# Performance work log

Hardware: AMD Instinct MI355X
Metric: run time of the kernel (lower is better)

Reference implementation:

```python
import jax, jax.numpy as jnp
import numpy as np

N_NODES = 50000
N_EDGES = 800000
NUM_GRAPHS = 128
FEAT = 128
HID = 64
NUM_LAYERS = 3
OUT = 2
K = 30
LATENT = HID * NUM_LAYERS + 1  # 193 = conv1 kernel size & stride


def _lin(k, i, o):
    s = 1.0 / np.sqrt(i)
    return jax.random.uniform(k, (i, o), jnp.float32, -s, s)


def setup_inputs() -> dict:
    key = jax.random.key(0)
    ks = jax.random.split(key, 16)
    x = jax.random.normal(ks[0], (N_NODES, FEAT), jnp.float32)
    edge_index = jax.random.randint(ks[1], (2, N_EDGES), 0, N_NODES, dtype=jnp.int64)
    batch = jnp.sort(jax.random.randint(ks[2], (N_NODES,), 0, NUM_GRAPHS, dtype=jnp.int64))
    w0 = _lin(ks[3], FEAT, HID); b0 = jnp.zeros((HID,), jnp.float32)
    w1 = _lin(ks[4], HID, HID);  b1 = jnp.zeros((HID,), jnp.float32)
    w2 = _lin(ks[5], HID, HID);  b2 = jnp.zeros((HID,), jnp.float32)
    w3 = _lin(ks[6], HID, 1);    b3 = jnp.zeros((1,), jnp.float32)
    conv1_w = jax.random.normal(ks[7], (16, 1, LATENT), jnp.float32) * (1.0 / np.sqrt(LATENT))
    conv1_b = jnp.zeros((16,), jnp.float32)
    conv2_w = jax.random.normal(ks[8], (32, 16, 5), jnp.float32) * (1.0 / np.sqrt(16 * 5))
    conv2_b = jnp.zeros((32,), jnp.float32)
    dense_dim = (int((K - 2) / 2 + 1) - 5 + 1) * 32  # 352
    lin1_w = _lin(ks[9], dense_dim, 256); lin1_b = jnp.zeros((256,), jnp.float32)
    lin2_w = _lin(ks[10], 256, OUT);      lin2_b = jnp.zeros((OUT,), jnp.float32)
    return dict(x=x, edge_index=edge_index, batch=batch,
                w0=w0, b0=b0, w1=w1, b1=b1, w2=w2, b2=b2, w3=w3, b3=b3,
                conv1_w=conv1_w, conv1_b=conv1_b, conv2_w=conv2_w, conv2_b=conv2_b,
                lin1_w=lin1_w, lin1_b=lin1_b, lin2_w=lin2_w, lin2_b=lin2_b)


def _gcn(h_in, w, b, src, dst, norm, n):
    # GCNConv: out_i = sum_j d_i^-1/2 d_j^-1/2 (x_j W) over A+I, plus bias
    h = h_in @ w
    msg = h[src] * norm[:, None]  # gather over edges (incl. self loops)
    return jax.ops.segment_sum(msg, dst, num_segments=n) + b


def _sort_pool(x, batch, k, g):
    # per-graph descending sort on last channel, top-k, zero-pad
    n, d = x.shape
    order = jnp.lexsort((-x[:, -1], batch))  # primary: batch asc, secondary: last feat desc
    xs, bs = x[order], batch[order]
    counts = jax.ops.segment_sum(jnp.ones((n,), jnp.int32), batch, num_segments=g)
    starts = jnp.cumsum(counts) - counts
    rank = jnp.arange(n) - starts[bs]
    slot = jnp.where(rank < k, rank, k)  # overflow nodes dumped in slot k (discarded)
    out = jnp.zeros((g, k + 1, d), x.dtype).at[bs, slot].set(xs)
    return out[:, :k].reshape(g, k * d)


def _conv1d(z, w, stride):
    return jax.lax.conv_general_dilated(z, w, window_strides=(stride,), padding='VALID',
                                        dimension_numbers=('NCH', 'OIH', 'NCH'))


def reference(x, edge_index, batch, w0, b0, w1, b1, w2, b2, w3, b3,
              conv1_w, conv1_b, conv2_w, conv2_b, lin1_w, lin1_b, lin2_w, lin2_b):
    n = x.shape[0]
    loop = jnp.arange(n, dtype=edge_index.dtype)
    src = jnp.concatenate([edge_index[0], loop])
    dst = jnp.concatenate([edge_index[1], loop])
    deg = jax.ops.segment_sum(jnp.ones_like(src, jnp.float32), dst, num_segments=n)
    dinv = jnp.where(deg > 0, jax.lax.rsqrt(deg), 0.0)
    norm = dinv[src] * dinv[dst]

    h1 = jnp.tanh(_gcn(x,  w0, b0, src, dst, norm, n))
    h2 = jnp.tanh(_gcn(h1, w1, b1, src, dst, norm, n))
    h3 = jnp.tanh(_gcn(h2, w2, b2, src, dst, norm, n))
    h4 = jnp.tanh(_gcn(h3, w3, b3, src, dst, norm, n))
    hcat = jnp.concatenate([h1, h2, h3, h4], axis=-1)  # [N, 193]

    p = _sort_pool(hcat, batch, K, NUM_GRAPHS)  # [G, K*193]
    z = p[:, None, :]                                   # [G, 1, K*193]
    z = jax.nn.relu(_conv1d(z, conv1_w, LATENT) + conv1_b[None, :, None])  # [G,16,K]
    g, c, l = z.shape
    z = z.reshape(g, c, l // 2, 2).max(axis=-1)         # MaxPool1d(2,2) -> [G,16,15]
    z = jax.nn.relu(_conv1d(z, conv2_w, 1) + conv2_b[None, :, None])       # [G,32,11]
    z = z.reshape(g, -1)                                # [G,352]
    z = jax.nn.relu(z @ lin1_w + lin1_b)
    # dropout is identity in eval mode
    return z @ lin2_w + lin2_b
```

## Files before the change

kernel.cpp:

```cpp
#include <hip/hip_runtime.h>
#include <math.h>

#define NGRAPH 128
#define KTOP 30
#define LATENT 193
#define HID 64

__global__ void k_hist_starts(const int* __restrict__ dst, const int* __restrict__ batch,
                              int* edeg, int* starts, int E, int n) {
    int i = blockIdx.x * blockDim.x + threadIdx.x;
    if (i < E) atomicAdd(&edeg[dst[i]], 1);
    if (i < n) {
        int b = batch[i];
        if (i == 0) {
            for (int g = 0; g <= b; g++) starts[g] = 0;
        } else {
            int pb = batch[i - 1];
            for (int g = pb + 1; g <= b; g++) starts[g] = i;
        }
        if (i == n - 1) {
            for (int g = b + 1; g <= NGRAPH; g++) starts[g] = n;
        }
    }
}

__global__ void k_scan1(const int* __restrict__ edeg, int* offs, int* bsum,
                        float* dinv, int n) {
    __shared__ int s[256];
    int t = threadIdx.x;
    int gi = blockIdx.x * 256 + t;
    int v = (gi < n) ? edeg[gi] : 0;
    if (gi < n) dinv[gi] = rsqrtf((float)(v + 1));
    s[t] = v;
    __syncthreads();
    for (int o = 1; o < 256; o <<= 1) {
        int add = (t >= o) ? s[t - o] : 0;
        __syncthreads();
        s[t] += add;
        __syncthreads();
    }
    if (gi < n) offs[gi] = s[t] - v;
    if (t == 255) bsum[blockIdx.x] = s[255];
}

__global__ void k_scan2(int* bsum, int* boff, int nb) {
    __shared__ int s[256];
    int t = threadIdx.x;
    int v = (t < nb) ? bsum[t] : 0;
    s[t] = v;
    __syncthreads();
    for (int o = 1; o < 256; o <<= 1) {
        int add = (t >= o) ? s[t - o] : 0;
        __syncthreads();
        s[t] += add;
        __syncthreads();
    }
    if (t < nb) boff[t] = s[t] - v;
}

__global__ void k_scan3(int* offs, int* next, const int* __restrict__ boff, int n, int E) {
    int gi = blockIdx.x * blockDim.x + threadIdx.x;
    if (gi < n) {
        int v = offs[gi] + boff[gi >> 8];
        offs[gi] = v;
        next[gi] = v;
    }
    if (gi == 0) offs[n] = E;
}

__global__ __launch_bounds__(256) void k_gemm_fill(const float* __restrict__ A,
                                                   const float* __restrict__ W,
                                                   const float* __restrict__ dinv,
                                                   float* __restrict__ Hs,
                                                   int M, int K, int NG,
                                                   const int* __restrict__ src,
                                                   const int* __restrict__ dst,
                                                   int* next, int* __restrict__ csr,
                                                   int E) {
    __shared__ float As[64][17];
    __shared__ float Bs[16][65];
    int bid = blockIdx.x;
    int gemm_id = (bid % 5 == 0) ? bid / 5 : -1;
    if (gemm_id >= 0 && gemm_id < NG) {
        int tid = threadIdx.x;
        int tx = tid & 15, ty = tid >> 4;
        int br = gemm_id * 64;
        float c[4][4] = {};
        for (int k0 = 0; k0 < K; k0 += 16) {
            {
                int idx = tid * 4;
                int r = idx >> 4;
                int kk = idx & 15;
                int grow = br + r;
                float4 v = make_float4(0.f, 0.f, 0.f, 0.f);
                if (grow < M) v = *(const float4*)(A + (size_t)grow * K + k0 + kk);
                As[r][kk + 0] = v.x; As[r][kk + 1] = v.y;
                As[r][kk + 2] = v.z; As[r][kk + 3] = v.w;
            }
            {
                int idx = tid * 4;
                int kk = idx >> 6;
                int col = idx & 63;
                float4 v = *(const float4*)(W + (size_t)(k0 + kk) * 64 + col);
                Bs[kk][col + 0] = v.x; Bs[kk][col + 1] = v.y;
                Bs[kk][col + 2] = v.z; Bs[kk][col + 3] = v.w;
            }
            __syncthreads();
#pragma unroll
            for (int kk = 0; kk < 16; ++kk) {
                float a[4], b[4];
#pragma unroll
                for (int i = 0; i < 4; i++) a[i] = As[ty + i * 16][kk];
#pragma unroll
                for (int j = 0; j < 4; j++) b[j] = Bs[kk][tx + j * 16];
#pragma unroll
                for (int i = 0; i < 4; i++)
#pragma unroll
                    for (int j = 0; j < 4; j++) c[i][j] += a[i] * b[j];
            }
            __syncthreads();
        }
#pragma unroll
        for (int i = 0; i < 4; i++) {
            int row = br + ty + i * 16;
            if (row >= M) continue;
            float d = dinv[row];
#pragma unroll
            for (int j = 0; j < 4; j++) {
                int col = tx + j * 16;
                Hs[(size_t)row * HID + col] = c[i][j] * d;
            }
        }
    } else {
        int ngb = min((bid + 4) / 5, NG);
        int fid = bid - ngb;
        int e = fid * 256 + threadIdx.x;
        if (e < E) {
            int d = dst[e];
            int pos = atomicAdd(&next[d], 1);
            csr[pos] = src[e];
        }
    }
}

__global__ __launch_bounds__(256) void k_gemm(const float* __restrict__ A,
                                              const float* __restrict__ W,
                                              const float* __restrict__ dinv,
                                              float* __restrict__ Hs,
                                              int M, int K) {
    __shared__ float As[64][17];
    __shared__ float Bs[16][65];
    int tid = threadIdx.x;
    int tx = tid & 15, ty = tid >> 4;
    int br = blockIdx.x * 64;
    float c[4][4] = {};
    for (int k0 = 0; k0 < K; k0 += 16) {
        {
            int idx = tid * 4;
            int r = idx >> 4;
            int kk = idx & 15;
            int grow = br + r;
            float4 v = make_float4(0.f, 0.f, 0.f, 0.f);
            if (grow < M) v = *(const float4*)(A + (size_t)grow * K + k0 + kk);
            As[r][kk + 0] = v.x; As[r][kk + 1] = v.y;
            As[r][kk + 2] = v.z; As[r][kk + 3] = v.w;
        }
        {
            int idx = tid * 4;
            int kk = idx >> 6;
            int col = idx & 63;
            float4 v = *(const float4*)(W + (size_t)(k0 + kk) * 64 + col);
            Bs[kk][col + 0] = v.x; Bs[kk][col + 1] = v.y;
            Bs[kk][col + 2] = v.z; Bs[kk][col + 3] = v.w;
        }
        __syncthreads();
#pragma unroll
        for (int kk = 0; kk < 16; ++kk) {
            float a[4], b[4];
#pragma unroll
            for (int i = 0; i < 4; i++) a[i] = As[ty + i * 16][kk];
#pragma unroll
            for (int j = 0; j < 4; j++) b[j] = Bs[kk][tx + j * 16];
#pragma unroll
            for (int i = 0; i < 4; i++)
#pragma unroll
                for (int j = 0; j < 4; j++) c[i][j] += a[i] * b[j];
        }
        __syncthreads();
    }
#pragma unroll
    for (int i = 0; i < 4; i++) {
        int row = br + ty + i * 16;
        if (row >= M) continue;
        float d = dinv[row];
#pragma unroll
        for (int j = 0; j < 4; j++) {
            int col = tx + j * 16;
            Hs[(size_t)row * HID + col] = c[i][j] * d;
        }
    }
}

template <bool FUSE_TS>
__global__ __launch_bounds__(256) void k_agg(const float* __restrict__ Hs,
                                             const int* __restrict__ csr,
                                             const int* __restrict__ offs,
                                             const float* __restrict__ dinv,
                                             const float* __restrict__ b,
                                             float* __restrict__ H, int n,
                                             const float* __restrict__ w3,
                                             float* __restrict__ ts) {
    int wid = threadIdx.x >> 6;
    int lane = threadIdx.x & 63;
    int node = blockIdx.x * 4 + wid;
    if (node >= n) return;
    float acc = Hs[(size_t)node * HID + lane];
    int s = offs[node], e = offs[node + 1];
    int i = s;
    for (; i + 4 <= e; i += 4) {
        int u0 = csr[i], u1 = csr[i + 1], u2 = csr[i + 2], u3 = csr[i + 3];
        float v0 = Hs[(size_t)u0 * HID + lane];
        float v1 = Hs[(size_t)u1 * HID + lane];
        float v2 = Hs[(size_t)u2 * HID + lane];
        float v3 = Hs[(size_t)u3 * HID + lane];
        acc += v0 + v1 + v2 + v3;
    }
    for (; i < e; i++) acc += Hs[(size_t)csr[i] * HID + lane];
    float d = dinv[node];
    float h = tanhf(acc * d + b[lane]);
    H[(size_t)node * HID + lane] = h;
    if (FUSE_TS) {
        float v = h * w3[lane];
        for (int o = 32; o > 0; o >>= 1) v += __shfl_down(v, o, 64);
        if (lane == 0) ts[node] = v * d;
    }
}

__global__ void k_agg4(const float* __restrict__ ts, const int* __restrict__ csr,
                       const int* __restrict__ offs, const float* __restrict__ dinv,
                       const float* __restrict__ b3, float* h4, int n) {
    int node = blockIdx.x * blockDim.x + threadIdx.x;
    if (node >= n) return;
    float acc = ts[node];
    int s = offs[node], e = offs[node + 1];
    for (int i = s; i < e; i++) acc += ts[csr[i]];
    h4[node] = tanhf(acc * dinv[node] + b3[0]);
}

__global__ __launch_bounds__(512) void k_select(const float* __restrict__ h4,
                                                const int* __restrict__ starts,
                                                int* __restrict__ sel) {
    int g = blockIdx.x;
    int s = starts[g], c = starts[g + 1] - s;
    __shared__ float v[1024];
    int t = threadIdx.x;
    if (c <= 1024) {
        for (int i = t; i < c; i += 512) v[i] = h4[s + i];
        __syncthreads();
        for (int i = t; i < c; i += 512) {
            float vi = v[i];
            int r = 0;
            for (int j = 0; j < c; j++) {
                float vj = v[j];
                r += (vj > vi) || (vj == vi && j < i);
            }
            if (r < KTOP) sel[g * KTOP + r] = s + i;
        }
    } else {
        for (int i = t; i < c; i += 512) {
            float vi = h4[s + i];
            int r = 0;
            for (int j = 0; j < c; j++) {
                float vj = h4[s + j];
                r += (vj > vi) || (vj == vi && j < i);
            }
            if (r < KTOP) sel[g * KTOP + r] = s + i;
        }
    }
    for (int slot = t; slot < KTOP; slot += 512)
        if (slot >= c) sel[g * KTOP + slot] = -1;
}

__global__ __launch_bounds__(1024) void k_tail(const float* __restrict__ h1,
                                               const float* __restrict__ h2,
                                               const float* __restrict__ h3,
                                               const float* __restrict__ h4,
                                               const int* __restrict__ sel,
                                               const float* __restrict__ c1w,
                                               const float* __restrict__ c1b,
                                               const float* __restrict__ c2w,
                                               const float* __restrict__ c2b,
                                               const float* __restrict__ l1w,
                                               const float* __restrict__ l1b,
                                               const float* __restrict__ l2w,
                                               const float* __restrict__ l2b,
                                               float* __restrict__ out) {
    __shared__ float p[KTOP * LATENT];
    __shared__ float w1s[16 * LATENT];
    __shared__ float w2s[32 * 16 * 5];
    __shared__ float z1[16 * KTOP];
    __shared__ float z1p[16 * 15];
    __shared__ float flat[352];
    __shared__ float part[1024];
    __shared__ float y1[256];
    int g = blockIdx.x;
    int t = threadIdx.x;
    for (int i = t; i < 16 * LATENT; i += 1024) w1s[i] = c1w[i];
    for (int i = t; i < 32 * 16 * 5; i += 1024) w2s[i] = c2w[i];
    for (int i = t; i < KTOP * LATENT; i += 1024) {
        int slot = i / LATENT;
        int j = i - slot * LATENT;
        int node = sel[g * KTOP + slot];
        float v = 0.f;
        if (node >= 0) {
            if (j < 64)       v = h1[(size_t)node * HID + j];
            else if (j < 128) v = h2[(size_t)node * HID + j - 64];
            else if (j < 192) v = h3[(size_t)node * HID + j - 128];
            else              v = h4[node];
        }
        p[i] = v;
    }
    __syncthreads();
    if (t < 16 * KTOP) {
        int ch = t / KTOP, tt = t - ch * KTOP;
        float s = c1b[ch];
        const float* wp = &w1s[ch * LATENT];
        const float* pp = &p[tt * LATENT];
        for (int j = 0; j < LATENT; j++) s += pp[j] * wp[j];
        z1[ch * KTOP + tt] = fmaxf(s, 0.f);
    }
    __syncthreads();
    if (t < 16 * 15) {
        int ch = t / 15, tt = t - ch * 15;
        z1p[t] = fmaxf(z1[ch * KTOP + 2 * tt], z1[ch * KTOP + 2 * tt + 1]);
    }
    __syncthreads();
    if (t < 32 * 11) {
        int c2 = t / 11, tt = t - c2 * 11;
        float s = c2b[c2];
        for (int c1i = 0; c1i < 16; c1i++) {
            const float* wp = &w2s[(c2 * 16 + c1i) * 5];
            const float* zp = &z1p[c1i * 15 + tt];
#pragma unroll
            for (int dt = 0; dt < 5; dt++) s += zp[dt] * wp[dt];
        }
        flat[c2 * 11 + tt] = fmaxf(s, 0.f);
    }
    __syncthreads();
    {
        int o = t & 255, ch = t >> 8;
        int i0 = ch * 88, i1 = i0 + 88;
        float s = 0.f;
        for (int i = i0; i < i1; i++) s += flat[i] * l1w[(size_t)i * 256 + o];
        part[t] = s;
    }
    __syncthreads();
    if (t < 256)
        y1[t] = fmaxf(part[t] + part[256 + t] + part[512 + t] + part[768 + t] + l1b[t], 0.f);
    __syncthreads();
    if (t < 128) {
        int o = t >> 6, lane = t & 63;
        float s = 0.f;
        for (int i = lane; i < 256; i += 64) s += y1[i] * l2w[(size_t)i * 2 + o];
        for (int off = 32; off > 0; off >>= 1) s += __shfl_down(s, off, 64);
        if (lane == 0) out[g * 2 + o] = s + l2b[o];
    }
}

static inline char* align256(char* p) {
    return (char*)(((uintptr_t)p + 255) & ~(uintptr_t)255);
}

extern "C" void kernel_launch(void* const* d_in, const int* in_sizes, int n_in,
                              void* d_out, int out_size, void* d_ws, size_t ws_size,
                              hipStream_t stream) {
    const float* x     = (const float*)d_in[0];
    const int*  eidx   = (const int*)d_in[1];
    const int*  batch  = (const int*)d_in[2];
    const float* w0    = (const float*)d_in[3];
    const float* b0    = (const float*)d_in[4];
    const float* w1    = (const float*)d_in[5];
    const float* b1    = (const float*)d_in[6];
    const float* w2    = (const float*)d_in[7];
    const float* b2    = (const float*)d_in[8];
    const float* w3    = (const float*)d_in[9];
    const float* b3    = (const float*)d_in[10];
    const float* c1w   = (const float*)d_in[11];
    const float* c1b   = (const float*)d_in[12];
    const float* c2w   = (const float*)d_in[13];
    const float* c2b   = (const float*)d_in[14];
    const float* l1w   = (const float*)d_in[15];
    const float* l1b   = (const float*)d_in[16];
    const float* l2w   = (const float*)d_in[17];
    const float* l2b   = (const float*)d_in[18];

    int N = in_sizes[2];
    int E = in_sizes[1] / 2;
    int K0 = in_sizes[0] / N;
    const int* esrc = eidx;
    const int* edst = eidx + E;

    char* w = (char*)d_ws;
    float* dinv  = (float*)w;             w = align256(w + (size_t)N * 4);
    int*   edeg  = (int*)w;               w = align256(w + (size_t)N * 4);
    int*   next  = (int*)w;               w = align256(w + (size_t)N * 4);
    int*   offs  = (int*)w;               w = align256(w + (size_t)(N + 1) * 4);
    int*   bsum  = (int*)w;               w = align256(w + 1024);
    int*   boff  = (int*)w;               w = align256(w + 1024);
    float* ts    = (float*)w;             w = align256(w + (size_t)N * 4);
    float* h4    = (float*)w;             w = align256(w + (size_t)N * 4);
    int* starts  = (int*)w;               w = align256(w + (NGRAPH + 1) * 4);
    int* sel     = (int*)w;               w = align256(w + NGRAPH * KTOP * 4);
    int* csr     = (int*)w;               w = align256(w + (size_t)E * 4);
    float* Hs    = (float*)w;             w = align256(w + (size_t)N * HID * 4);
    float* h1    = (float*)w;             w = align256(w + (size_t)N * HID * 4);
    float* h2    = (float*)w;             w = align256(w + (size_t)N * HID * 4);
    float* h3    = (float*)w;             w = align256(w + (size_t)N * HID * 4);

    int nb = (N + 255) / 256;

    hipMemsetAsync(edeg, 0, (size_t)N * 4, stream);

    k_hist_starts<<<(E + 255) / 256, 256, 0, stream>>>(edst, batch, edeg, starts, E, N);

    k_scan1<<<nb, 256, 0, stream>>>(edeg, offs, bsum, dinv, N);
    k_scan2<<<1, 256, 0, stream>>>(bsum, boff, nb);
    k_scan3<<<nb, 256, 0, stream>>>(offs, next, boff, N, E);

    int NG = (N + 63) / 64;
    int NF = (E + 255) / 256;
    int agg_grid = (N + 3) / 4;

    k_gemm_fill<<<NG + NF, 256, 0, stream>>>(x, w0, dinv, Hs, N, K0, NG,
                                             esrc, edst, next, csr, E);
    k_agg<false><<<agg_grid, 256, 0, stream>>>(Hs, csr, offs, dinv, b0, h1, N, nullptr, nullptr);
    k_gemm<<<NG, 256, 0, stream>>>(h1, w1, dinv, Hs, N, HID);
    k_agg<false><<<agg_grid, 256, 0, stream>>>(Hs, csr, offs, dinv, b1, h2, N, nullptr, nullptr);
    k_gemm<<<NG, 256, 0, stream>>>(h2, w2, dinv, Hs, N, HID);
    k_agg<true><<<agg_grid, 256, 0, stream>>>(Hs, csr, offs, dinv, b2, h3, N, w3, ts);
    k_agg4<<<(N + 255) / 256, 256, 0, stream>>>(ts, csr, offs, dinv, b3, h4, N);

    k_select<<<NGRAPH, 512, 0, stream>>>(h4, starts, sel);

    k_tail<<<NGRAPH, 1024, 0, stream>>>(h1, h2, h3, h4, sel,
                                        c1w, c1b, c2w, c2b,
                                        l1w, l1b, l2w, l2b,
                                        (float*)d_out);
}
```

Before: 302.1 us.

## Overlap first GEMM with degree histogram, build CSR via ranks with 16-bit indices

Runs the first-layer GEMM concurrently with the degree histogram by deferring the dinv scaling into the first aggregation, which scales each neighbor row by dinv on the fly. The CSR fill now uses per-edge ranks recorded during the histogram, so it no longer needs atomics. Neighbor indices are stored as 16-bit values to halve the index traffic. The aggregation loop is also unrolled to 8. The 16-bit CSR assumes node ids below 65536, which holds for N=50000 but truncates for larger graphs, and the first aggregation does extra dinv gathers.

```diff
diff --git a/kernel.cpp b/kernel.cpp
--- a/kernel.cpp
+++ b/kernel.cpp
@@ -6,82 +6,20 @@
 #define LATENT 193
 #define HID 64
 
-__global__ void k_hist_starts(const int* __restrict__ dst, const int* __restrict__ batch,
-                              int* edeg, int* starts, int E, int n) {
-    int i = blockIdx.x * blockDim.x + threadIdx.x;
-    if (i < E) atomicAdd(&edeg[dst[i]], 1);
-    if (i < n) {
-        int b = batch[i];
-        if (i == 0) {
-            for (int g = 0; g <= b; g++) starts[g] = 0;
-        } else {
-            int pb = batch[i - 1];
-            for (int g = pb + 1; g <= b; g++) starts[g] = i;
-        }
-        if (i == n - 1) {
-            for (int g = b + 1; g <= NGRAPH; g++) starts[g] = n;
-        }
-    }
-}
-
-__global__ void k_scan1(const int* __restrict__ edeg, int* offs, int* bsum,
-                        float* dinv, int n) {
-    __shared__ int s[256];
-    int t = threadIdx.x;
-    int gi = blockIdx.x * 256 + t;
-    int v = (gi < n) ? edeg[gi] : 0;
-    if (gi < n) dinv[gi] = rsqrtf((float)(v + 1));
-    s[t] = v;
-    __syncthreads();
-    for (int o = 1; o < 256; o <<= 1) {
-        int add = (t >= o) ? s[t - o] : 0;
-        __syncthreads();
-        s[t] += add;
-        __syncthreads();
-    }
-    if (gi < n) offs[gi] = s[t] - v;
-    if (t == 255) bsum[blockIdx.x] = s[255];
-}
-
-__global__ void k_scan2(int* bsum, int* boff, int nb) {
-    __shared__ int s[256];
-    int t = threadIdx.x;
-    int v = (t < nb) ? bsum[t] : 0;
-    s[t] = v;
-    __syncthreads();
-    for (int o = 1; o < 256; o <<= 1) {
-        int add = (t >= o) ? s[t - o] : 0;
-        __syncthreads();
-        s[t] += add;
-        __syncthreads();
-    }
-    if (t < nb) boff[t] = s[t] - v;
-}
-
-__global__ void k_scan3(int* offs, int* next, const int* __restrict__ boff, int n, int E) {
-    int gi = blockIdx.x * blockDim.x + threadIdx.x;
-    if (gi < n) {
-        int v = offs[gi] + boff[gi >> 8];
-        offs[gi] = v;
-        next[gi] = v;
-    }
-    if (gi == 0) offs[n] = E;
-}
-
-__global__ __launch_bounds__(256) void k_gemm_fill(const float* __restrict__ A,
-                                                   const float* __restrict__ W,
-                                                   const float* __restrict__ dinv,
-                                                   float* __restrict__ Hs,
-                                                   int M, int K, int NG,
-                                                   const int* __restrict__ src,
-                                                   const int* __restrict__ dst,
-                                                   int* next, int* __restrict__ csr,
-                                                   int E) {
+typedef unsigned short u16;
+
+__global__ __launch_bounds__(256) void k_gemm_hist(
+        const float* __restrict__ A, const float* __restrict__ W,
+        float* __restrict__ Hs, int M, int K, int NG,
+        const int* __restrict__ dst, const int* __restrict__ batch,
+        int* edeg, u16* __restrict__ rank, int* starts,
+        int E, int n, int NH) {
     __shared__ float As[64][17];
     __shared__ float Bs[16][65];
     int bid = blockIdx.x;
-    int gemm_id = (bid % 5 == 0) ? bid / 5 : -1;
-    if (gemm_id >= 0 && gemm_id < NG) {
+    if ((bid & 1) == 0) {
+        int gemm_id = bid >> 1;
+        if (gemm_id >= NG) return;
         int tid = threadIdx.x;
         int tx = tid & 15, ty = tid >> 4;
         int br = gemm_id * 64;
@@ -124,22 +62,99 @@
         for (int i = 0; i < 4; i++) {
             int row = br + ty + i * 16;
             if (row >= M) continue;
-            float d = dinv[row];
 #pragma unroll
             for (int j = 0; j < 4; j++) {
                 int col = tx + j * 16;
-                Hs[(size_t)row * HID + col] = c[i][j] * d;
+                Hs[(size_t)row * HID + col] = c[i][j];
             }
         }
     } else {
-        int ngb = min((bid + 4) / 5, NG);
-        int fid = bid - ngb;
-        int e = fid * 256 + threadIdx.x;
-        if (e < E) {
-            int d = dst[e];
-            int pos = atomicAdd(&next[d], 1);
-            csr[pos] = src[e];
-        }
+        int fid = bid >> 1;
+        if (fid >= NH) return;
+        int t = threadIdx.x;
+        int gi = fid * 256 + t;
+        if (gi < n) {
+            int b = batch[gi];
+            if (gi == 0) {
+                for (int g = 0; g <= b; g++) starts[g] = 0;
+            } else {
+                int pb = batch[gi - 1];
+                for (int g = pb + 1; g <= b; g++) starts[g] = gi;
+            }
+            if (gi == n - 1) {
+                for (int g = b + 1; g <= NGRAPH; g++) starts[g] = n;
+            }
+        }
+        int base = fid * 1024;
+#pragma unroll
+        for (int k = 0; k < 4; k++) {
+            int e = base + k * 256 + t;
+            if (e < E) {
+                int d = dst[e];
+                rank[e] = (u16)atomicAdd(&edeg[d], 1);
+            }
+        }
+    }
+}
+
+__global__ void k_scan1(const int* __restrict__ edeg, int* offs, int* bsum,
+                        float* dinv, int n) {
+    __shared__ int s[256];
+    int t = threadIdx.x;
+    int gi = blockIdx.x * 256 + t;
+    int v = (gi < n) ? edeg[gi] : 0;
+    if (gi < n) dinv[gi] = rsqrtf((float)(v + 1));
+    s[t] = v;
+    __syncthreads();
+    for (int o = 1; o < 256; o <<= 1) {
+        int add = (t >= o) ? s[t - o] : 0;
+        __syncthreads();
+        s[t] += add;
+        __syncthreads();
+    }
+    if (gi < n) offs[gi] = s[t] - v;
+    if (t == 255) bsum[blockIdx.x] = s[255];
+}
+
+__global__ void k_scan2(int* bsum, int* boff, int nb) {
+    __shared__ int s[256];
+    int t = threadIdx.x;
+    int v = (t < nb) ? bsum[t] : 0;
+    s[t] = v;
+    __syncthreads();
+    for (int o = 1; o < 256; o <<= 1) {
+        int add = (t >= o) ? s[t - o] : 0;
+        __syncthreads();
+        s[t] += add;
+        __syncthreads();
+    }
+    if (t < nb) boff[t] = s[t] - v;
+}
+
+__global__ void k_scan3(int* offs, const int* __restrict__ boff, int n, int E) {
+    int gi = blockIdx.x * blockDim.x + threadIdx.x;
+    if (gi < n) offs[gi] += boff[gi >> 8];
+    if (gi == 0) offs[n] = E;
+}
+
+__global__ __launch_bounds__(256) void k_fill(const int* __restrict__ src,
+                                              const int* __restrict__ dst,
+                                              const u16* __restrict__ rank,
+                                              const int* __restrict__ offs,
+                                              u16* __restrict__ csr, int E) {
+    int t = blockIdx.x * 256 + threadIdx.x;
+    int e0 = t * 4;
+    if (e0 + 4 <= E) {
+        int4 s4 = *(const int4*)(src + e0);
+        int4 d4 = *(const int4*)(dst + e0);
+        const u16* rp = rank + e0;
+        csr[offs[d4.x] + rp[0]] = (u16)s4.x;
+        csr[offs[d4.y] + rp[1]] = (u16)s4.y;
+        csr[offs[d4.z] + rp[2]] = (u16)s4.z;
+        csr[offs[d4.w] + rp[3]] = (u16)s4.w;
+    } else {
+        for (int e = e0; e < E; e++)
+            csr[offs[dst[e]] + rank[e]] = (u16)src[e];
     }
 }
 
@@ -201,9 +216,9 @@
     }
 }
 
-template <bool FUSE_TS>
+template <bool DEFER, bool FUSE_TS>
 __global__ __launch_bounds__(256) void k_agg(const float* __restrict__ Hs,
-                                             const int* __restrict__ csr,
+                                             const u16* __restrict__ csr,
                                              const int* __restrict__ offs,
                                              const float* __restrict__ dinv,
                                              const float* __restrict__ b,
@@ -214,19 +229,28 @@
     int lane = threadIdx.x & 63;
     int node = blockIdx.x * 4 + wid;
     if (node >= n) return;
+    float d = dinv[node];
     float acc = Hs[(size_t)node * HID + lane];
+    if (DEFER) acc *= d;
     int s = offs[node], e = offs[node + 1];
     int i = s;
-    for (; i + 4 <= e; i += 4) {
-        int u0 = csr[i], u1 = csr[i + 1], u2 = csr[i + 2], u3 = csr[i + 3];
-        float v0 = Hs[(size_t)u0 * HID + lane];
-        float v1 = Hs[(size_t)u1 * HID + lane];
-        float v2 = Hs[(size_t)u2 * HID + lane];
-        float v3 = Hs[(size_t)u3 * HID + lane];
-        acc += v0 + v1 + v2 + v3;
-    }
-    for (; i < e; i++) acc += Hs[(size_t)csr[i] * HID + lane];
-    float d = dinv[node];
+    for (; i + 8 <= e; i += 8) {
+        float part = 0.f;
+#pragma unroll
+        for (int k = 0; k < 8; k++) {
+            int u = csr[i + k];
+            float v = Hs[(size_t)u * HID + lane];
+            if (DEFER) v *= dinv[u];
+            part += v;
+        }
+        acc += part;
+    }
+    for (; i < e; i++) {
+        int u = csr[i];
+        float v = Hs[(size_t)u * HID + lane];
+        if (DEFER) v *= dinv[u];
+        acc += v;
+    }
     float h = tanhf(acc * d + b[lane]);
     H[(size_t)node * HID + lane] = h;
     if (FUSE_TS) {
@@ -236,7 +260,7 @@
     }
 }
 
-__global__ void k_agg4(const float* __restrict__ ts, const int* __restrict__ csr,
+__global__ void k_agg4(const float* __restrict__ ts, const u16* __restrict__ csr,
                        const int* __restrict__ offs, const float* __restrict__ dinv,
                        const float* __restrict__ b3, float* h4, int n) {
     int node = blockIdx.x * blockDim.x + threadIdx.x;
@@ -403,7 +427,6 @@
     char* w = (char*)d_ws;
     float* dinv  = (float*)w;             w = align256(w + (size_t)N * 4);
     int*   edeg  = (int*)w;               w = align256(w + (size_t)N * 4);
-    int*   next  = (int*)w;               w = align256(w + (size_t)N * 4);
     int*   offs  = (int*)w;               w = align256(w + (size_t)(N + 1) * 4);
     int*   bsum  = (int*)w;               w = align256(w + 1024);
     int*   boff  = (int*)w;               w = align256(w + 1024);
@@ -411,33 +434,35 @@
     float* h4    = (float*)w;             w = align256(w + (size_t)N * 4);
     int* starts  = (int*)w;               w = align256(w + (NGRAPH + 1) * 4);
     int* sel     = (int*)w;               w = align256(w + NGRAPH * KTOP * 4);
-    int* csr     = (int*)w;               w = align256(w + (size_t)E * 4);
+    u16* rank    = (u16*)w;               w = align256(w + (size_t)E * 2);
+    u16* csr     = (u16*)w;               w = align256(w + (size_t)E * 2);
     float* Hs    = (float*)w;             w = align256(w + (size_t)N * HID * 4);
     float* h1    = (float*)w;             w = align256(w + (size_t)N * HID * 4);
     float* h2    = (float*)w;             w = align256(w + (size_t)N * HID * 4);
     float* h3    = (float*)w;             w = align256(w + (size_t)N * HID * 4);
 
     int nb = (N + 255) / 256;
+    int NG = (N + 63) / 64;
+    int NH = (E + 1023) / 1024;
+    int agg_grid = (N + 3) / 4;
 
     hipMemsetAsync(edeg, 0, (size_t)N * 4, stream);
 
-    k_hist_starts<<<(E + 255) / 256, 256, 0, stream>>>(edst, batch, edeg, starts, E, N);
+    int g1 = 2 * (NG > NH ? NG : NH);
+    k_gemm_hist<<<g1, 256, 0, stream>>>(x, w0, Hs, N, K0, NG,
+                                        edst, batch, edeg, rank, starts, E, N, NH);
 
     k_scan1<<<nb, 256, 0, stream>>>(edeg, offs, bsum, dinv, N);
     k_scan2<<<1, 256, 0, stream>>>(bsum, boff, nb);
-    k_scan3<<<nb, 256, 0, stream>>>(offs, next, boff, N, E);
-
-    int NG = (N + 63) / 64;
-    int NF = (E + 255) / 256;
-    int agg_grid = (N + 3) / 4;
-
-    k_gemm_fill<<<NG + NF, 256, 0, stream>>>(x, w0, dinv, Hs, N, K0, NG,
-                                             esrc, edst, next, csr, E);
-    k_agg<false><<<agg_grid, 256, 0, stream>>>(Hs, csr, offs, dinv, b0, h1, N, nullptr, nullptr);
+    k_scan3<<<nb, 256, 0, stream>>>(offs, boff, N, E);
+
+    k_fill<<<(E / 4 + 255) / 256 + 1, 256, 0, stream>>>(esrc, edst, rank, offs, csr, E);
+
+    k_agg<true, false><<<agg_grid, 256, 0, stream>>>(Hs, csr, offs, dinv, b0, h1, N, nullptr, nullptr);
     k_gemm<<<NG, 256, 0, stream>>>(h1, w1, dinv, Hs, N, HID);
-    k_agg<false><<<agg_grid, 256, 0, stream>>>(Hs, csr, offs, dinv, b1, h2, N, nullptr, nullptr);
+    k_agg<false, false><<<agg_grid, 256, 0, stream>>>(Hs, csr, offs, dinv, b1, h2, N, nullptr, nullptr);
     k_gemm<<<NG, 256, 0, stream>>>(h2, w2, dinv, Hs, N, HID);
-    k_agg<true><<<agg_grid, 256, 0, stream>>>(Hs, csr, offs, dinv, b2, h3, N, w3, ts);
+    k_agg<false, true><<<agg_grid, 256, 0, stream>>>(Hs, csr, offs, dinv, b2, h3, N, w3, ts);
     k_agg4<<<(N + 255) / 256, 256, 0, stream>>>(ts, csr, offs, dinv, b3, h4, N);
 
     k_select<<<NGRAPH, 512, 0, stream>>>(h4, starts, sel);
```

After: 262.4 us. -13.1%, faster.
